# Optimization experiments

Measured on AMD Instinct MI355X. Metric: run time of the kernel, lower is better.

The kernel has to match this reference:

```python
import jax, jax.numpy as jnp
import numpy as np

DILATIONS = (1, 4, 16)

def setup_inputs() -> dict:
    key = jax.random.key(0)
    k1, _ = jax.random.split(key)
    B, C, H, W = 4, 64, 512, 512
    u = jax.random.normal(k1, (B, C, H, W), dtype=jnp.float32)
    # matches nn.Parameter(torch.ones(len(dilations), channels) * 0.1)
    D = jnp.full((len(DILATIONS), C), 0.1, dtype=jnp.float32)
    return {"u": u, "D": D}

def _lap5(u, d):
    # 5-point stencil at dilation d with replicate (edge) boundary:
    # u(x+d,y)+u(x-d,y)+u(x,y+d)+u(x,y-d)-4u(x,y)
    p = jnp.pad(u, ((0, 0), (0, 0), (d, d), (d, d)), mode='edge')
    H, W = u.shape[-2], u.shape[-1]
    up    = p[:, :, :H,     d:d+W]
    down  = p[:, :, 2*d:,   d:d+W]
    left  = p[:, :, d:d+H,  :W]
    right = p[:, :, d:d+H,  2*d:]
    return up + down + left + right - 4.0 * u

def reference(u, D):
    out = jnp.zeros_like(u)
    for i, d in enumerate(DILATIONS):
        scale = jax.nn.softplus(D[i])[None, :, None, None]  # (1,C,1,1)
        out = out + scale * _lap5(u, d)
    return out
```

## Files before the change

### kernel.cpp

```cpp
#include <hip/hip_runtime.h>
#include <math.h>

#define HH 512
#define WW 512
#define W4 128
#define IMG (HH * WW)

typedef float f32x4 __attribute__((ext_vector_type(4)));

__device__ __forceinline__ f32x4 bc4(float v) { f32x4 r = {v, v, v, v}; return r; }

__device__ __forceinline__ float softplus(float x) {
    return fmaxf(x, 0.0f) + log1pf(expf(-fabsf(x)));
}

template<bool CLAMP>
__device__ __forceinline__ void compute_tile(const f32x4* __restrict__ img4,
                                             f32x4* __restrict__ out4,
                                             int h0, int q,
                                             float s0, float s1, float s2, float m4c)
{
    auto ld = [&](int r) -> f32x4 {
        const int rr = CLAMP ? (r < 0 ? 0 : (r > HH - 1 ? HH - 1 : r)) : r;
        return img4[rr * W4 + q];
    };

    f32x4 C[6];
#pragma unroll
    for (int k = 0; k < 6; ++k) C[k] = ld(h0 - 1 + k);
    f32x4 U4[3], D4[3];
#pragma unroll
    for (int k = 0; k < 3; ++k) U4[k] = ld(h0 - 4 + k);
#pragma unroll
    for (int k = 0; k < 3; ++k) D4[k] = ld(h0 + 5 + k);
    f32x4 U16[4], D16[4];
#pragma unroll
    for (int k = 0; k < 4; ++k) U16[k] = ld(h0 - 16 + k);
#pragma unroll
    for (int k = 0; k < 4; ++k) D16[k] = ld(h0 + 16 + k);

    const int qm1 = max(q - 1, 0), qp1 = min(q + 1, W4 - 1);
    const int qm4 = max(q - 4, 0), qp4 = min(q + 4, W4 - 1);
    const bool pl4 = (q == 0), pr4 = (q == W4 - 1);
    const bool pl16 = (q < 4), pr16 = (q > W4 - 5);

#pragma unroll
    for (int r = 0; r < 4; ++r) {
        const int rr = h0 + r;
        const f32x4* __restrict__ rowq = img4 + rr * W4;

        f32x4 l4 = rowq[qm1];  if (pl4)  l4 = bc4(l4.x);
        f32x4 r4 = rowq[qp1];  if (pr4)  r4 = bc4(r4.w);
        f32x4 l16 = rowq[qm4]; if (pl16) l16 = bc4(l16.x);
        f32x4 r16 = rowq[qp4]; if (pr16) r16 = bc4(r16.w);

        const f32x4 cc  = C[r + 1];
        const f32x4 up1 = C[r], dn1 = C[r + 2];
        const f32x4 up4 = (r < 3) ? U4[r] : C[0];
        const f32x4 dn4 = (r == 0) ? C[5] : D4[r - 1];
        const f32x4 u16v = U16[r], d16v = D16[r];

        f32x4 l1 = { l4.w, cc.x, cc.y, cc.z };
        f32x4 r1 = { cc.y, cc.z, cc.w, r4.x };

        const f32x4 d1s  = (up1 + dn1) + (l1 + r1);
        const f32x4 d4s  = (up4 + dn4) + (l4 + r4);
        const f32x4 d16s = (u16v + d16v) + (l16 + r16);

        f32x4 o;
#pragma unroll
        for (int j = 0; j < 4; ++j) {
            float acc = m4c * cc[j];
            acc = fmaf(s0, d1s[j], acc);
            acc = fmaf(s1, d4s[j], acc);
            acc = fmaf(s2, d16s[j], acc);
            o[j] = acc;
        }
        __builtin_nontemporal_store(o, out4 + rr * W4 + q);
    }
}

__global__ __launch_bounds__(256) void lap3_kernel(const float* __restrict__ u,
                                                   const float* __restrict__ D,
                                                   float* __restrict__ out) {
    const int bid = blockIdx.x;
    const int b2  = (bid & 7) * 256 + (bid >> 3);
    const int q   = threadIdx.x & 127;
    const int sub = threadIdx.x >> 7;

    const int c0 = (b2 >> 6) & 63;
    const int c1 = (c0 + 32) & 63;
    const float sA0 = softplus(D[c0]), sA1 = softplus(D[64 + c0]), sA2 = softplus(D[128 + c0]);
    const float sB0 = softplus(D[c1]), sB1 = softplus(D[64 + c1]), sB2 = softplus(D[128 + c1]);

#pragma unroll 1
    for (int it = 0; it < 8; ++it) {
        const int s  = b2 + it * 2048;
        const int bc = s >> 6;
        const int h0 = ((s & 63) << 3) + (sub << 2);

        const float t0 = (it & 1) ? sB0 : sA0;
        const float t1 = (it & 1) ? sB1 : sA1;
        const float t2 = (it & 1) ? sB2 : sA2;
        const float m4c = -4.0f * (t0 + t1 + t2);

        const f32x4* img4 = reinterpret_cast<const f32x4*>(u) + (size_t)bc * (IMG / 4);
        f32x4* out4 = reinterpret_cast<f32x4*>(out) + (size_t)bc * (IMG / 4);

        if (h0 >= 16 && h0 <= HH - 20)
            compute_tile<false>(img4, out4, h0, q, t0, t1, t2, m4c);
        else
            compute_tile<true>(img4, out4, h0, q, t0, t1, t2, m4c);
    }
}

extern "C" void kernel_launch(void* const* d_in, const int* in_sizes, int n_in,
                              void* d_out, int out_size, void* d_ws, size_t ws_size,
                              hipStream_t stream) {
    const float* u = (const float*)d_in[0];
    const float* D = (const float*)d_in[1];
    float* out = (float*)d_out;

    lap3_kernel<<<2048, 256, 0, stream>>>(u, D, out);
}
```

Baseline: 105.8 us.

## Stream image halves through an LDS ring buffer with register-prefetched staging

```diff
diff --git a/kernel.cpp b/kernel.cpp
--- a/kernel.cpp
+++ b/kernel.cpp
@@ -3,114 +3,133 @@
 
 #define HH 512
 #define WW 512
-#define W4 128
+#define W4Q 128
 #define IMG (HH * WW)
+#define NR 64
+#define RST 129
+#define SS 32
+#define HALF 256
 
 typedef float f32x4 __attribute__((ext_vector_type(4)));
 
 __device__ __forceinline__ f32x4 bc4(float v) { f32x4 r = {v, v, v, v}; return r; }
-
 __device__ __forceinline__ float softplus(float x) {
     return fmaxf(x, 0.0f) + log1pf(expf(-fabsf(x)));
 }
 
-template<bool CLAMP>
-__device__ __forceinline__ void compute_tile(const f32x4* __restrict__ img4,
-                                             f32x4* __restrict__ out4,
-                                             int h0, int q,
-                                             float s0, float s1, float s2, float m4c)
-{
-    auto ld = [&](int r) -> f32x4 {
-        const int rr = CLAMP ? (r < 0 ? 0 : (r > HH - 1 ? HH - 1 : r)) : r;
-        return img4[rr * W4 + q];
-    };
+__global__ __launch_bounds__(512, 2) void lap3_kernel(const float* __restrict__ u,
+                                                      const float* __restrict__ D,
+                                                      float* __restrict__ out) {
+    __shared__ f32x4 lds[NR * RST];
 
-    f32x4 C[6];
-#pragma unroll
-    for (int k = 0; k < 6; ++k) C[k] = ld(h0 - 1 + k);
-    f32x4 U4[3], D4[3];
-#pragma unroll
-    for (int k = 0; k < 3; ++k) U4[k] = ld(h0 - 4 + k);
-#pragma unroll
-    for (int k = 0; k < 3; ++k) D4[k] = ld(h0 + 5 + k);
-    f32x4 U16[4], D16[4];
-#pragma unroll
-    for (int k = 0; k < 4; ++k) U16[k] = ld(h0 - 16 + k);
-#pragma unroll
-    for (int k = 0; k < 4; ++k) D16[k] = ld(h0 + 16 + k);
+    const int b    = blockIdx.x;
+    const int bc   = b >> 1;
+    const int row0 = (b & 1) * HALF;
+    const int c    = bc & 63;
 
-    const int qm1 = max(q - 1, 0), qp1 = min(q + 1, W4 - 1);
-    const int qm4 = max(q - 4, 0), qp4 = min(q + 4, W4 - 1);
-    const bool pl4 = (q == 0), pr4 = (q == W4 - 1);
-    const bool pl16 = (q < 4), pr16 = (q > W4 - 5);
+    const float s0 = softplus(D[c]);
+    const float s1 = softplus(D[64 + c]);
+    const float s2 = softplus(D[128 + c]);
+    const float m4c = -4.0f * (s0 + s1 + s2);
+
+    const int t  = threadIdx.x;
+    const int q  = t & 127;
+    const int g  = t >> 7;
+    const int sc = t & 15;
+    const int sr = t >> 4;
+
+    const f32x4* __restrict__ img4 =
+        reinterpret_cast<const f32x4*>(u) + (size_t)bc * (IMG / 4);
+    f32x4* __restrict__ out4 =
+        reinterpret_cast<f32x4*>(out) + (size_t)bc * (IMG / 4);
 
 #pragma unroll
-    for (int r = 0; r < 4; ++r) {
-        const int rr = h0 + r;
-        const f32x4* __restrict__ rowq = img4 + rr * W4;
+    for (int rnd = 0; rnd < 2; ++rnd) {
+        const int vrow = row0 - 16 + rnd * 32 + sr;
+        const int crow = min(max(vrow, 0), HH - 1);
+        const int slot = vrow & (NR - 1);
+#pragma unroll
+        for (int j = 0; j < 8; ++j) {
+            const int qc = sc + 16 * j;
+            lds[slot * RST + qc] = img4[crow * W4Q + qc];
+        }
+    }
+    __syncthreads();
 
-        f32x4 l4 = rowq[qm1];  if (pl4)  l4 = bc4(l4.x);
-        f32x4 r4 = rowq[qp1];  if (pr4)  r4 = bc4(r4.w);
-        f32x4 l16 = rowq[qm4]; if (pl16) l16 = bc4(l16.x);
-        f32x4 r16 = rowq[qp4]; if (pr16) r16 = bc4(r16.w);
-
-        const f32x4 cc  = C[r + 1];
-        const f32x4 up1 = C[r], dn1 = C[r + 2];
-        const f32x4 up4 = (r < 3) ? U4[r] : C[0];
-        const f32x4 dn4 = (r == 0) ? C[5] : D4[r - 1];
-        const f32x4 u16v = U16[r], d16v = D16[r];
-
-        f32x4 l1 = { l4.w, cc.x, cc.y, cc.z };
-        f32x4 r1 = { cc.y, cc.z, cc.w, r4.x };
-
-        const f32x4 d1s  = (up1 + dn1) + (l1 + r1);
-        const f32x4 d4s  = (up4 + dn4) + (l4 + r4);
-        const f32x4 d16s = (u16v + d16v) + (l16 + r16);
-
-        f32x4 o;
-#pragma unroll
-        for (int j = 0; j < 4; ++j) {
-            float acc = m4c * cc[j];
-            acc = fmaf(s0, d1s[j], acc);
-            acc = fmaf(s1, d4s[j], acc);
-            acc = fmaf(s2, d16s[j], acc);
-            o[j] = acc;
-        }
-        __builtin_nontemporal_store(o, out4 + rr * W4 + q);
-    }
-}
-
-__global__ __launch_bounds__(256) void lap3_kernel(const float* __restrict__ u,
-                                                   const float* __restrict__ D,
-                                                   float* __restrict__ out) {
-    const int bid = blockIdx.x;
-    const int b2  = (bid & 7) * 256 + (bid >> 3);
-    const int q   = threadIdx.x & 127;
-    const int sub = threadIdx.x >> 7;
-
-    const int c0 = (b2 >> 6) & 63;
-    const int c1 = (c0 + 32) & 63;
-    const float sA0 = softplus(D[c0]), sA1 = softplus(D[64 + c0]), sA2 = softplus(D[128 + c0]);
-    const float sB0 = softplus(D[c1]), sB1 = softplus(D[64 + c1]), sB2 = softplus(D[128 + c1]);
+    const int qm1 = max(q - 1, 0), qp1 = min(q + 1, W4Q - 1);
+    const int qm4 = max(q - 4, 0), qp4 = min(q + 4, W4Q - 1);
+    const bool pl4 = (q == 0), pr4 = (q == W4Q - 1);
+    const bool pl16 = (q < 4), pr16 = (q > W4Q - 5);
 
 #pragma unroll 1
-    for (int it = 0; it < 8; ++it) {
-        const int s  = b2 + it * 2048;
-        const int bc = s >> 6;
-        const int h0 = ((s & 63) << 3) + (sub << 2);
+    for (int step = 0; step < HALF / SS; ++step) {
+        const int h0 = row0 + step * SS;
 
-        const float t0 = (it & 1) ? sB0 : sA0;
-        const float t1 = (it & 1) ? sB1 : sA1;
-        const float t2 = (it & 1) ? sB2 : sA2;
-        const float m4c = -4.0f * (t0 + t1 + t2);
+        f32x4 gbuf[8];
+        int nslot = 0;
+        const bool do_stage = (step + 1 < HALF / SS);
+        if (do_stage) {
+            const int vrow = h0 + 48 + sr;
+            const int crow = min(vrow, HH - 1);
+            nslot = vrow & (NR - 1);
+#pragma unroll
+            for (int j = 0; j < 8; ++j)
+                gbuf[j] = img4[crow * W4Q + sc + 16 * j];
+        }
 
-        const f32x4* img4 = reinterpret_cast<const f32x4*>(u) + (size_t)bc * (IMG / 4);
-        f32x4* out4 = reinterpret_cast<f32x4*>(out) + (size_t)bc * (IMG / 4);
+        const int hr = h0 + g * 8;
+        f32x4 C[10];
+#pragma unroll
+        for (int k = 0; k < 10; ++k)
+            C[k] = lds[((hr - 1 + k) & (NR - 1)) * RST + q];
+        f32x4 U4[3], D4v[3];
+#pragma unroll
+        for (int k = 0; k < 3; ++k)
+            U4[k] = lds[((hr - 4 + k) & (NR - 1)) * RST + q];
+#pragma unroll
+        for (int k = 0; k < 3; ++k)
+            D4v[k] = lds[((hr + 9 + k) & (NR - 1)) * RST + q];
 
-        if (h0 >= 16 && h0 <= HH - 20)
-            compute_tile<false>(img4, out4, h0, q, t0, t1, t2, m4c);
-        else
-            compute_tile<true>(img4, out4, h0, q, t0, t1, t2, m4c);
+#pragma unroll
+        for (int r = 0; r < 8; ++r) {
+            const int rs = ((hr + r) & (NR - 1)) * RST;
+            f32x4 l4 = lds[rs + qm1];  if (pl4)  l4 = bc4(l4.x);
+            f32x4 r4 = lds[rs + qp1];  if (pr4)  r4 = bc4(r4.w);
+            f32x4 l16 = lds[rs + qm4]; if (pl16) l16 = bc4(l16.x);
+            f32x4 r16 = lds[rs + qp4]; if (pr16) r16 = bc4(r16.w);
+            const f32x4 u16 = lds[((hr + r - 16) & (NR - 1)) * RST + q];
+            const f32x4 d16 = lds[((hr + r + 16) & (NR - 1)) * RST + q];
+
+            const f32x4 cc = C[r + 1], up1 = C[r], dn1 = C[r + 2];
+            const f32x4 u4 = (r < 3) ? U4[r] : C[r - 3];
+            const f32x4 d4 = (r > 4) ? D4v[r - 5] : C[r + 5];
+
+            f32x4 l1 = { l4.w, cc.x, cc.y, cc.z };
+            f32x4 r1 = { cc.y, cc.z, cc.w, r4.x };
+
+            const f32x4 d1s  = (up1 + dn1) + (l1 + r1);
+            const f32x4 d4s  = (u4 + d4) + (l4 + r4);
+            const f32x4 d16s = (u16 + d16) + (l16 + r16);
+
+            f32x4 o;
+#pragma unroll
+            for (int j = 0; j < 4; ++j) {
+                float acc = m4c * cc[j];
+                acc = fmaf(s0, d1s[j], acc);
+                acc = fmaf(s1, d4s[j], acc);
+                acc = fmaf(s2, d16s[j], acc);
+                o[j] = acc;
+            }
+            __builtin_nontemporal_store(o, out4 + (hr + r) * W4Q + q);
+        }
+
+        __syncthreads();
+        if (do_stage) {
+#pragma unroll
+            for (int j = 0; j < 8; ++j)
+                lds[nslot * RST + sc + 16 * j] = gbuf[j];
+        }
+        __syncthreads();
     }
 }
 
@@ -121,5 +140,5 @@
     const float* D = (const float*)d_in[1];
     float* out = (float*)d_out;
 
-    lap3_kernel<<<2048, 256, 0, stream>>>(u, D, out);
+    lap3_kernel<<<512, 512, 0, stream>>>(u, D, out);
 }
```

Result: faster. 87.75 us (-17.1%).
